# Kernel tuning notes

Hardware: AMD Instinct MI355X
Metric: run time of the kernel (lower is better)

The kernel has to match this reference:

```python
import jax, jax.numpy as jnp
import numpy as np
from jax import lax

ALPHA = 0.3  # SSGConv alpha


def _cdist(x):
    # Euclidean distance matrix [N, N] for x: [N, H]
    n2 = jnp.sum(x * x, axis=-1)
    d2 = n2[:, None] + n2[None, :] - 2.0 * (x @ x.T)
    return jnp.sqrt(jnp.maximum(d2, 0.0))


def _prim(dist):
    # Dense O(N^2) Prim MST starting at node 0. Returns (parents, children, weights), each [N-1].
    N = dist.shape[0]
    INF = jnp.float32(1e30)
    in_tree = jnp.zeros(N, dtype=bool).at[0].set(True)
    mind = dist[0]                       # best edge weight into tree per node
    parent = jnp.zeros(N, dtype=jnp.int32)

    def step(carry, _):
        in_tree, mind, parent = carry
        d = jnp.where(in_tree, INF, mind)
        v = jnp.argmin(d).astype(jnp.int32)
        w = d[v]
        p = parent[v]
        in_tree = in_tree.at[v].set(True)
        newd = dist[v]
        upd = newd < mind
        mind = jnp.where(upd, newd, mind)
        parent = jnp.where(upd, v, parent)
        return (in_tree, mind, parent), (p, v, w)

    _, (ps, vs, ws) = lax.scan(step, (in_tree, mind, parent), None, length=N - 1)
    return ps, vs, ws


def _build_edges(features):
    # Torch code detaches edge weights via .item(); mirror with stop_gradient.
    B, N, _ = features.shape
    dist = jax.vmap(_cdist)(lax.stop_gradient(features))   # [B, N, N]
    ps, vs, ws = jax.vmap(_prim)(dist)                     # each [B, N-1]
    off = (jnp.arange(B, dtype=jnp.int32) * N)[:, None]
    a = (ps + off).ravel()
    b = (vs + off).ravel()
    src = jnp.concatenate([a, b])   # MST edges are added in both directions
    dst = jnp.concatenate([b, a])
    ew = jnp.concatenate([ws.ravel(), ws.ravel()])
    return src, dst, ew


def _gcn_norm(src, dst, ew, num_nodes):
    # PyG gcn_norm: add self loops (weight 1), symmetric deg^-1/2 normalization.
    loop = jnp.arange(num_nodes, dtype=src.dtype)
    src = jnp.concatenate([src, loop])
    dst = jnp.concatenate([dst, loop])
    ew = jnp.concatenate([ew, jnp.ones(num_nodes, ew.dtype)])
    deg = jax.ops.segment_sum(ew, dst, num_segments=num_nodes)
    dinv = jnp.where(deg > 0, lax.rsqrt(jnp.maximum(deg, 1e-30)), 0.0)
    norm = dinv[src] * ew * dinv[dst]
    return src, dst, norm


def _ssg_conv(x, src, dst, norm, W, b, num_nodes):
    # SSGConv with K=1: h = alpha*x + (1-alpha)*A_hat x, then linear.
    prop = jax.ops.segment_sum(norm[:, None] * x[src], dst, num_segments=num_nodes)
    h = ALPHA * x + (1.0 - ALPHA) * prop
    return h @ W + b


def _forward(features, W1, b1, W2, b2, W3, b3, Wd, bd, Wo, bo):
    B, N, H = features.shape
    NT = B * N
    src, dst, ew = _build_edges(features)
    src, dst, norm = _gcn_norm(src, dst, ew, NT)
    x = features.reshape(NT, H)
    x = jnp.tanh(_ssg_conv(x, src, dst, norm, W1, b1, NT))
    x = jnp.tanh(_ssg_conv(x, src, dst, norm, W2, b2, NT))
    x = jnp.tanh(_ssg_conv(x, src, dst, norm, W3, b3, NT))
    # dropout: eval mode -> identity. global_mean_pool: each graph has exactly N nodes.
    pooled = x.reshape(B, N, -1).mean(axis=1)          # [B, 2H]
    h = jnp.tanh(pooled @ Wd + bd)                     # [B, H]
    return h @ Wo + bo                                 # [B, num_labels]


def setup_inputs() -> dict:
    key = jax.random.key(0)
    ks = jax.random.split(key, 12)
    B, N, H, L = 16, 1024, 256, 8
    H2 = 2 * H

    def lin(k, fin, fout):
        s = 1.0 / np.sqrt(fin)
        k1, k2 = jax.random.split(k)
        return (jax.random.uniform(k1, (fin, fout), jnp.float32, -s, s),
                jax.random.uniform(k2, (fout,), jnp.float32, -s, s))

    W1, b1 = lin(ks[1], H, H2)
    W2, b2 = lin(ks[2], H2, H2)
    W3, b3 = lin(ks[3], H2, H2)
    Wd, bd = lin(ks[4], H2, H)
    Wo, bo = lin(ks[5], H, L)
    features = jax.random.normal(ks[0], (B, N, H), jnp.float32)
    return {"features": features, "W1": W1, "b1": b1, "W2": W2, "b2": b2,
            "W3": W3, "b3": b3, "Wd": Wd, "bd": bd, "Wo": Wo, "bo": bo}


def reference(features, W1, b1, W2, b2, W3, b3, Wd, bd, Wo, bo):
    return _forward(features, W1, b1, W2, b2, W3, b3, Wd, bd, Wo, bo)
```

## Files before the change

### kernel.cpp

```cpp
#include <hip/hip_runtime.h>
#include <math.h>

namespace {

constexpr float ALPHA = 0.3f;
constexpr int B  = 16;
constexpr int N  = 1024;
constexpr int H  = 256;
constexpr int H2 = 512;
constexpr int NT = B * N;
constexpr int NE = N - 1;
constexpr int CAP = 32;

__device__ __forceinline__ unsigned umin32(unsigned a, unsigned b) { return a < b ? a : b; }

typedef __attribute__((ext_vector_type(8))) short short8;
typedef __attribute__((ext_vector_type(4))) float f32x4;

__global__ void n2_kernel(const float* __restrict__ x, float* __restrict__ n2) {
  int wave = threadIdx.x >> 6, lane = threadIdx.x & 63;
  int row  = blockIdx.x * 4 + wave;
  float4 v = *(const float4*)(x + (size_t)row * H + lane * 4);
  float s  = v.x * v.x + v.y * v.y + v.z * v.z + v.w * v.w;
  #pragma unroll
  for (int off = 32; off; off >>= 1) s += __shfl_xor(s, off);
  if (lane == 0) n2[row] = s;
}

__global__ __launch_bounds__(256) void dist_kernel(const float* __restrict__ x,
    const float* __restrict__ n2, float* __restrict__ dist) {
  __shared__ float As[16][132], Bs[16][132];
  const int bb = blockIdx.z;
  int idx = blockIdx.x, ti = 0;
  while (idx >= 8 - ti) { idx -= 8 - ti; ++ti; }
  const int tj = ti + idx;
  const int i0 = ti * 128, j0 = tj * 128;
  const int t = threadIdx.x, tx = t & 15, ty = t >> 4;
  const float* xb = x + (size_t)bb * N * H;
  float acc[8][8] = {};
  for (int kc = 0; kc < H; kc += 16) {
    #pragma unroll
    for (int u = 0; u < 2; ++u) {
      int q = t + u * 256;
      int row = q >> 2, kf = (q & 3) * 4;
      float4 a = *(const float4*)(xb + (size_t)(i0 + row) * H + kc + kf);
      As[kf + 0][row] = a.x; As[kf + 1][row] = a.y;
      As[kf + 2][row] = a.z; As[kf + 3][row] = a.w;
      float4 bv = *(const float4*)(xb + (size_t)(j0 + row) * H + kc + kf);
      Bs[kf + 0][row] = bv.x; Bs[kf + 1][row] = bv.y;
      Bs[kf + 2][row] = bv.z; Bs[kf + 3][row] = bv.w;
    }
    __syncthreads();
    #pragma unroll
    for (int kk = 0; kk < 16; ++kk) {
      float4 a0 = *(const float4*)&As[kk][ty * 4];
      float4 a1 = *(const float4*)&As[kk][64 + ty * 4];
      float4 b0 = *(const float4*)&Bs[kk][tx * 4];
      float4 b1 = *(const float4*)&Bs[kk][64 + tx * 4];
      float ar[8] = {a0.x,a0.y,a0.z,a0.w,a1.x,a1.y,a1.z,a1.w};
      float br[8] = {b0.x,b0.y,b0.z,b0.w,b1.x,b1.y,b1.z,b1.w};
      #pragma unroll
      for (int r = 0; r < 8; ++r)
        #pragma unroll
        for (int c = 0; c < 8; ++c) acc[r][c] += ar[r] * br[c];
    }
    __syncthreads();
  }
  float n2i[8], n2j[8];
  #pragma unroll
  for (int r = 0; r < 8; ++r)
    n2i[r] = n2[bb * N + i0 + (r < 4 ? ty * 4 + r : 64 + ty * 4 + r - 4)];
  #pragma unroll
  for (int c = 0; c < 8; ++c)
    n2j[c] = n2[bb * N + j0 + (c < 4 ? tx * 4 + c : 64 + tx * 4 + c - 4)];
  const bool mirror = (ti != tj);
  float* distb = dist + (size_t)bb * N * N;
  #pragma unroll
  for (int r = 0; r < 8; ++r) {
    int mi = i0 + (r < 4 ? ty * 4 + r : 64 + ty * 4 + r - 4);
    float o[8];
    #pragma unroll
    for (int c = 0; c < 8; ++c) {
      float d2 = (n2i[r] + n2j[c]) - 2.0f * acc[r][c];
      o[c] = sqrtf(fmaxf(d2, 0.0f));
    }
    float* dst = distb + (size_t)mi * N + j0;
    *(float4*)(dst + tx * 4)      = make_float4(o[0], o[1], o[2], o[3]);
    *(float4*)(dst + 64 + tx * 4) = make_float4(o[4], o[5], o[6], o[7]);
    if (mirror) {
      #pragma unroll
      for (int c = 0; c < 8; ++c) {
        int mj = j0 + (c < 4 ? tx * 4 + c : 64 + tx * 4 + c - 4);
        distb[(size_t)mj * N + mi] = o[c];
      }
    }
  }
}

__device__ __forceinline__ unsigned wave_min_u32(unsigned x) {
  unsigned t;
  t = (unsigned)__builtin_amdgcn_update_dpp((int)x, (int)x, 0x111, 0xf, 0xf, false); x = umin32(x, t);
  t = (unsigned)__builtin_amdgcn_update_dpp((int)x, (int)x, 0x112, 0xf, 0xf, false); x = umin32(x, t);
  t = (unsigned)__builtin_amdgcn_update_dpp((int)x, (int)x, 0x114, 0xf, 0xf, false); x = umin32(x, t);
  t = (unsigned)__builtin_amdgcn_update_dpp((int)x, (int)x, 0x118, 0xf, 0xf, false); x = umin32(x, t);
  x = umin32(x, (unsigned)__shfl_xor((int)x, 16));
  x = umin32(x, (unsigned)__shfl_xor((int)x, 32));
  return (unsigned)__builtin_amdgcn_readlane((int)x, 63);
}

struct Sel2 { unsigned w; int j; };

__device__ __forceinline__ Sel2 block_select(unsigned mw0, unsigned mw1,
    unsigned mw2, unsigned mw3, int wid, int lane, unsigned long long* smin) {
  unsigned lm = umin32(umin32(mw0, mw1), umin32(mw2, mw3));
  unsigned wm = wave_min_u32(lm);
  unsigned mb = (mw0 == wm ? 1u : 0u) | (mw1 == wm ? 2u : 0u) |
                (mw2 == wm ? 4u : 0u) | (mw3 == wm ? 8u : 0u);
  unsigned long long bal = __ballot(mb != 0);
  int fl = __ffsll(bal) - 1;
  int slot = __ffs((unsigned)__builtin_amdgcn_readlane((int)mb, fl)) - 1;
  int widx = (wid << 8) | (fl << 2) | slot;
  if (lane == 0)
    smin[wid] = ((unsigned long long)wm << 32) | (unsigned)widx;
  __syncthreads();
  unsigned long long k0 = smin[0], k1 = smin[1], k2 = smin[2], k3 = smin[3];
  unsigned long long ka = k0 < k1 ? k0 : k1;
  unsigned long long kb = k2 < k3 ? k2 : k3;
  unsigned long long kk = ka < kb ? ka : kb;
  __syncthreads();
  Sel2 r; r.w = (unsigned)(kk >> 32); r.j = (int)(unsigned)(kk & 0xFFFFFFFFu);
  return r;
}

__global__ __launch_bounds__(256) void prim_gemm1_kernel(
    const float* __restrict__ dist, const float* __restrict__ feat,
    const float* __restrict__ W1, int* __restrict__ ep, int* __restrict__ ev,
    float* __restrict__ ewt, float* __restrict__ y) {
  __shared__ unsigned long long smin[4];
  __shared__ int epv[NE];
  __shared__ int evv[NE];
  __shared__ float ews[NE];
  __shared__ float As[16][132], Bs[16][132];
  if (blockIdx.x < B) {
    const int b = blockIdx.x;
    const int tid = threadIdx.x, wid = tid >> 6, lane = tid & 63;
    const float* Db = dist + (size_t)b * N * N;
    const int jbase = tid * 4;

    unsigned d0, d1, d2, d3;
    {
      float4 v = *(const float4*)(Db + jbase);
      d0 = __float_as_uint(v.x); d1 = __float_as_uint(v.y);
      d2 = __float_as_uint(v.z); d3 = __float_as_uint(v.w);
    }
    unsigned mw0 = d0, mw1 = d1, mw2 = d2, mw3 = d3;
    unsigned rm0 = 0, rm1 = 0, rm2 = 0, rm3 = 0;
    int pa0 = 0, pa1 = 0, pa2 = 0, pa3 = 0;
    if (tid == 0) { rm0 = ~0u; mw0 = ~0u; }

    Sel2 s0 = block_select(mw0, mw1, mw2, mw3, wid, lane, smin);
    int cj = s0.j;
    if ((cj >> 2) == tid) {
      int sl = cj & 3;
      int pv = pa0; if (sl == 1) pv = pa1; if (sl == 2) pv = pa2; if (sl == 3) pv = pa3;
      epv[0] = pv; evv[0] = cj; ews[0] = __uint_as_float(s0.w);
      if (sl == 0) { rm0 = ~0u; mw0 = ~0u; }
      if (sl == 1) { rm1 = ~0u; mw1 = ~0u; }
      if (sl == 2) { rm2 = ~0u; mw2 = ~0u; }
      if (sl == 3) { rm3 = ~0u; mw3 = ~0u; }
    }
    float4 xq = *(const float4*)(Db + (size_t)cj * N + jbase);

    for (int k = 1; k < NE; ++k) {
      unsigned r0 = __float_as_uint(xq.x), r1 = __float_as_uint(xq.y);
      unsigned r2 = __float_as_uint(xq.z), r3 = __float_as_uint(xq.w);
      unsigned q0 = r0 | rm0, q1 = r1 | rm1, q2 = r2 | rm2, q3 = r3 | rm3;
      mw0 = umin32(mw0, q0); mw1 = umin32(mw1, q1);
      mw2 = umin32(mw2, q2); mw3 = umin32(mw3, q3);
      Sel2 se = block_select(mw0, mw1, mw2, mw3, wid, lane, smin);
      const int nj = se.j;
      float4 nxt = *(const float4*)(Db + (size_t)nj * N + jbase);
      if (r0 < d0) { pa0 = cj; d0 = r0; }
      if (r1 < d1) { pa1 = cj; d1 = r1; }
      if (r2 < d2) { pa2 = cj; d2 = r2; }
      if (r3 < d3) { pa3 = cj; d3 = r3; }
      if ((nj >> 2) == tid) {
        int sl = nj & 3;
        int pv = pa0; if (sl == 1) pv = pa1; if (sl == 2) pv = pa2; if (sl == 3) pv = pa3;
        epv[k] = pv; evv[k] = nj; ews[k] = __uint_as_float(se.w);
        if (sl == 0) { rm0 = ~0u; mw0 = ~0u; }
        if (sl == 1) { rm1 = ~0u; mw1 = ~0u; }
        if (sl == 2) { rm2 = ~0u; mw2 = ~0u; }
        if (sl == 3) { rm3 = ~0u; mw3 = ~0u; }
      }
      cj = nj; xq = nxt;
    }

    __syncthreads();
    for (int e = tid; e < NE; e += 256) {
      ep[b * NE + e]  = epv[e];
      ev[b * NE + e]  = evv[e];
      ewt[b * NE + e] = ews[e];
    }
  } else {
    const int gb = blockIdx.x - B;
    const int m0 = (gb >> 2) * 128, n0 = (gb & 3) * 128;
    const int t = threadIdx.x, tx = t & 15, ty = t >> 4;
    float acc[8][8] = {};
    for (int kc = 0; kc < H; kc += 16) {
      #pragma unroll
      for (int u = 0; u < 2; ++u) {
        int q = t + u * 256;
        int row = q >> 2, kf = (q & 3) * 4;
        float4 a = *(const float4*)(feat + (size_t)(m0 + row) * H + kc + kf);
        As[kf + 0][row] = a.x; As[kf + 1][row] = a.y;
        As[kf + 2][row] = a.z; As[kf + 3][row] = a.w;
        int rowB = q >> 5, cf = (q & 31) * 4;
        *(float4*)&Bs[rowB][cf] = *(const float4*)(W1 + (size_t)(kc + rowB) * H2 + n0 + cf);
      }
      __syncthreads();
      #pragma unroll
      for (int kk = 0; kk < 16; ++kk) {
        float4 a0 = *(const float4*)&As[kk][ty * 4];
        float4 a1 = *(const float4*)&As[kk][64 + ty * 4];
        float4 b0 = *(const float4*)&Bs[kk][tx * 4];
        float4 b1 = *(const float4*)&Bs[kk][64 + tx * 4];
        float ar[8] = {a0.x,a0.y,a0.z,a0.w,a1.x,a1.y,a1.z,a1.w};
        float br[8] = {b0.x,b0.y,b0.z,b0.w,b1.x,b1.y,b1.z,b1.w};
        #pragma unroll
        for (int r = 0; r < 8; ++r)
          #pragma unroll
          for (int c = 0; c < 8; ++c) acc[r][c] += ar[r] * br[c];
      }
      __syncthreads();
    }
    #pragma unroll
    for (int r = 0; r < 8; ++r) {
      int m = m0 + (r < 4 ? ty * 4 + r : 64 + ty * 4 + r - 4);
      float* dst = y + (size_t)m * H2 + n0;
      *(float4*)(dst + tx * 4)      = make_float4(acc[r][0], acc[r][1], acc[r][2], acc[r][3]);
      *(float4*)(dst + 64 + tx * 4) = make_float4(acc[r][4], acc[r][5], acc[r][6], acc[r][7]);
    }
  }
}

__global__ void adj_kernel(const int* __restrict__ ep, const int* __restrict__ ev,
    const float* __restrict__ ewt, int* __restrict__ adjI, float* __restrict__ adjW,
    int* __restrict__ cnt, float* __restrict__ dinv) {
  int i = blockIdx.x * 256 + threadIdx.x;
  int b = i >> 10, loc = i & 1023;
  const int* epb = ep + b * NE;
  const int* evb = ev + b * NE;
  const float* ewb = ewt + b * NE;
  int c = 0; float wsum = 0.0f;
  for (int k = 0; k < NE; ++k) {
    int p = epb[k], v = evb[k];
    if (p == loc || v == loc) {
      float w = ewb[k];
      wsum += w;
      int nb = (p == loc) ? v : p;
      if (c < CAP) { adjI[i * CAP + c] = (b << 10) + nb; adjW[i * CAP + c] = w; }
      ++c;
    }
  }
  cnt[i]  = c < CAP ? c : CAP;
  dinv[i] = 1.0f / sqrtf(wsum + 1.0f);
}

__global__ void finish1_kernel(const float* __restrict__ y, const int* __restrict__ adjI,
    const float* __restrict__ adjW, const int* __restrict__ cnt,
    const float* __restrict__ dinv, const float* __restrict__ b1,
    float* __restrict__ out1) {
  int wave = threadIdx.x >> 6, lane = threadIdx.x & 63;
  int i = blockIdx.x * 4 + wave;
  float dv = dinv[i];
  int c = cnt[i];
  float selfc = ALPHA + (1.0f - ALPHA) * dv * dv;
  float4 acc[2];
  const float* yi = y + (size_t)i * H2 + lane * 4;
  #pragma unroll
  for (int u = 0; u < 2; ++u) {
    float4 v = *(const float4*)(yi + u * 256);
    acc[u].x = selfc * v.x; acc[u].y = selfc * v.y;
    acc[u].z = selfc * v.z; acc[u].w = selfc * v.w;
  }
  for (int e = 0; e < c; ++e) {
    int j   = adjI[i * CAP + e];
    float w = adjW[i * CAP + e];
    float coef = (1.0f - ALPHA) * dv * (w * dinv[j]);
    const float* yj = y + (size_t)j * H2 + lane * 4;
    #pragma unroll
    for (int u = 0; u < 2; ++u) {
      float4 v = *(const float4*)(yj + u * 256);
      acc[u].x += coef * v.x; acc[u].y += coef * v.y;
      acc[u].z += coef * v.z; acc[u].w += coef * v.w;
    }
  }
  float* ho = out1 + (size_t)i * H2 + lane * 4;
  #pragma unroll
  for (int u = 0; u < 2; ++u) {
    float4 bb = *(const float4*)(b1 + lane * 4 + u * 256);
    float4 o;
    o.x = tanhf(acc[u].x + bb.x); o.y = tanhf(acc[u].y + bb.y);
    o.z = tanhf(acc[u].z + bb.z); o.w = tanhf(acc[u].w + bb.w);
    *(float4*)(ho + u * 256) = o;
  }
}

template <int HH>
__global__ void prop_kernel(const float* __restrict__ x, const int* __restrict__ adjI,
    const float* __restrict__ adjW, const int* __restrict__ cnt,
    const float* __restrict__ dinv, float* __restrict__ h) {
  constexpr int U = HH / 256;
  int wave = threadIdx.x >> 6, lane = threadIdx.x & 63;
  int i = blockIdx.x * 4 + wave;
  float dv = dinv[i];
  int c = cnt[i];
  float selfc = ALPHA + (1.0f - ALPHA) * dv * dv;
  float4 acc[U];
  const float* xi = x + (size_t)i * HH + lane * 4;
  #pragma unroll
  for (int u = 0; u < U; ++u) {
    float4 v = *(const float4*)(xi + u * 256);
    acc[u].x = selfc * v.x; acc[u].y = selfc * v.y;
    acc[u].z = selfc * v.z; acc[u].w = selfc * v.w;
  }
  for (int e = 0; e < c; ++e) {
    int j   = adjI[i * CAP + e];
    float w = adjW[i * CAP + e];
    float coef = (1.0f - ALPHA) * dv * (w * dinv[j]);
    const float* xj = x + (size_t)j * HH + lane * 4;
    #pragma unroll
    for (int u = 0; u < U; ++u) {
      float4 v = *(const float4*)(xj + u * 256);
      acc[u].x += coef * v.x; acc[u].y += coef * v.y;
      acc[u].z += coef * v.z; acc[u].w += coef * v.w;
    }
  }
  float* ho = h + (size_t)i * HH + lane * 4;
  #pragma unroll
  for (int u = 0; u < U; ++u) *(float4*)(ho + u * 256) = acc[u];
}

__device__ __forceinline__ void bf16split(float a, unsigned short& hi, unsigned short& lo) {
  unsigned u = __float_as_uint(a);
  hi = (unsigned short)(u >> 16);
  float fh = __uint_as_float(u & 0xFFFF0000u);
  float fl = a - fh;
  lo = (unsigned short)(__float_as_uint(fl) >> 16);
}

__global__ __launch_bounds__(256) void mgemm_tanh_kernel(const float* __restrict__ A,
    const float* __restrict__ W, const float* __restrict__ bias, float* __restrict__ C) {
  __shared__ unsigned short Ahi[128][40], Alo[128][40];
  __shared__ unsigned short Bhi[128][40], Blo[128][40];
  const int m0 = blockIdx.x * 128, n0 = blockIdx.y * 128;
  const int t = threadIdx.x;
  const int w = t >> 6, lane = t & 63;
  const int lrow = lane & 15, lk = (lane >> 4) * 8;
  f32x4 acc[2][8];
  #pragma unroll
  for (int mt = 0; mt < 2; ++mt)
    #pragma unroll
    for (int nt = 0; nt < 8; ++nt) acc[mt][nt] = (f32x4){0.f, 0.f, 0.f, 0.f};

  const int arow = t >> 1, akq = (t & 1) * 16;
  const int wr = t & 31, wc4 = (t >> 5) * 16;

  for (int kc = 0; kc < H2; kc += 32) {
    {
      const float* src = A + (size_t)(m0 + arow) * H2 + kc + akq;
      unsigned short h[16], l[16];
      #pragma unroll
      for (int i = 0; i < 16; i += 4) {
        float4 v = *(const float4*)(src + i);
        bf16split(v.x, h[i], l[i]);     bf16split(v.y, h[i+1], l[i+1]);
        bf16split(v.z, h[i+2], l[i+2]); bf16split(v.w, h[i+3], l[i+3]);
      }
      short8 ph0 = {(short)h[0],(short)h[1],(short)h[2],(short)h[3],
                    (short)h[4],(short)h[5],(short)h[6],(short)h[7]};
      short8 ph1 = {(short)h[8],(short)h[9],(short)h[10],(short)h[11],
                    (short)h[12],(short)h[13],(short)h[14],(short)h[15]};
      short8 pl0 = {(short)l[0],(short)l[1],(short)l[2],(short)l[3],
                    (short)l[4],(short)l[5],(short)l[6],(short)l[7]};
      short8 pl1 = {(short)l[8],(short)l[9],(short)l[10],(short)l[11],
                    (short)l[12],(short)l[13],(short)l[14],(short)l[15]};
      *(short8*)&Ahi[arow][akq]     = ph0;
      *(short8*)&Ahi[arow][akq + 8] = ph1;
      *(short8*)&Alo[arow][akq]     = pl0;
      *(short8*)&Alo[arow][akq + 8] = pl1;
    }
    {
      const float* wsrc = W + (size_t)(kc + wr) * H2 + n0 + wc4;
      #pragma unroll
      for (int i = 0; i < 16; i += 4) {
        float4 v = *(const float4*)(wsrc + i);
        unsigned short h0,h1,h2,h3,l0,l1,l2,l3;
        bf16split(v.x, h0, l0); bf16split(v.y, h1, l1);
        bf16split(v.z, h2, l2); bf16split(v.w, h3, l3);
        Bhi[wc4+i+0][wr] = h0; Bhi[wc4+i+1][wr] = h1;
        Bhi[wc4+i+2][wr] = h2; Bhi[wc4+i+3][wr] = h3;
        Blo[wc4+i+0][wr] = l0; Blo[wc4+i+1][wr] = l1;
        Blo[wc4+i+2][wr] = l2; Blo[wc4+i+3][wr] = l3;
      }
    }
    __syncthreads();
    const int r0 = w * 32 + lrow;
    short8 a0h = *(const short8*)&Ahi[r0][lk];
    short8 a0l = *(const short8*)&Alo[r0][lk];
    short8 a1h = *(const short8*)&Ahi[r0 + 16][lk];
    short8 a1l = *(const short8*)&Alo[r0 + 16][lk];
    #pragma unroll
    for (int nt = 0; nt < 8; ++nt) {
      short8 bh = *(const short8*)&Bhi[nt * 16 + lrow][lk];
      short8 bl = *(const short8*)&Blo[nt * 16 + lrow][lk];
      acc[0][nt] = __builtin_amdgcn_mfma_f32_16x16x32_bf16(a0h, bh, acc[0][nt], 0, 0, 0);
      acc[0][nt] = __builtin_amdgcn_mfma_f32_16x16x32_bf16(a0l, bh, acc[0][nt], 0, 0, 0);
      acc[0][nt] = __builtin_amdgcn_mfma_f32_16x16x32_bf16(a0h, bl, acc[0][nt], 0, 0, 0);
      acc[1][nt] = __builtin_amdgcn_mfma_f32_16x16x32_bf16(a1h, bh, acc[1][nt], 0, 0, 0);
      acc[1][nt] = __builtin_amdgcn_mfma_f32_16x16x32_bf16(a1l, bh, acc[1][nt], 0, 0, 0);
      acc[1][nt] = __builtin_amdgcn_mfma_f32_16x16x32_bf16(a1h, bl, acc[1][nt], 0, 0, 0);
    }
    __syncthreads();
  }
  #pragma unroll
  for (int mt = 0; mt < 2; ++mt) {
    #pragma unroll
    for (int nt = 0; nt < 8; ++nt) {
      int col = n0 + nt * 16 + lrow;
      float bcol = bias[col];
      #pragma unroll
      for (int i = 0; i < 4; ++i) {
        int row = m0 + w * 32 + mt * 16 + (lane >> 4) * 4 + i;
        C[(size_t)row * H2 + col] = tanhf(acc[mt][nt][i] + bcol);
      }
    }
  }
}

__global__ void pool_kernel(const float* __restrict__ x, float* __restrict__ pooled) {
  int b = blockIdx.x;
  int c = blockIdx.y * 256 + threadIdx.x;
  const float* xb = x + ((size_t)b << 10) * H2 + c;
  float s = 0.0f;
  for (int i = 0; i < N; ++i) s += xb[(size_t)i * H2];
  pooled[b * H2 + c] = s * (1.0f / N);
}

__global__ void head_kernel(const float* __restrict__ pooled, const float* __restrict__ Wd,
    const float* __restrict__ bd, const float* __restrict__ Wo, const float* __restrict__ bo,
    float* __restrict__ out) {
  __shared__ float sp[512], sh[256];
  int b = blockIdx.x, t = threadIdx.x;
  sp[t] = pooled[b * H2 + t];
  sp[t + 256] = pooled[b * H2 + t + 256];
  __syncthreads();
  float acc = bd[t];
  for (int c2 = 0; c2 < 512; ++c2) acc += sp[c2] * Wd[c2 * 256 + t];
  sh[t] = tanhf(acc);
  __syncthreads();
  if (t < 8) {
    float o = bo[t];
    for (int j = 0; j < 256; ++j) o += sh[j] * Wo[j * 8 + t];
    out[b * 8 + t] = o;
  }
}

}

extern "C" void kernel_launch(void* const* d_in, const int* in_sizes, int n_in,
                              void* d_out, int out_size, void* d_ws, size_t ws_size,
                              hipStream_t stream) {
  const float* feat = (const float*)d_in[0];
  const float* W1 = (const float*)d_in[1];
  const float* b1 = (const float*)d_in[2];
  const float* W2 = (const float*)d_in[3];
  const float* b2 = (const float*)d_in[4];
  const float* W3 = (const float*)d_in[5];
  const float* b3 = (const float*)d_in[6];
  const float* Wd = (const float*)d_in[7];
  const float* bd = (const float*)d_in[8];
  const float* Wo = (const float*)d_in[9];
  const float* bo = (const float*)d_in[10];
  float* out = (float*)d_out;
  char* ws = (char*)d_ws;

  float* dist = (float*)(ws);
  float* out1 = (float*)(ws);
  float* x2   = (float*)(ws + ((size_t)32 << 20));
  float* x3   = (float*)(ws);
  float* ybuf = (float*)(ws + ((size_t)64 << 20));
  float* hbuf = (float*)(ws + ((size_t)64 << 20));
  char* misc  = ws + ((size_t)96 << 20);
  int*   ep     = (int*)(misc);
  int*   ev     = (int*)(misc + 65536);
  float* ewt    = (float*)(misc + 131072);
  int*   cnt    = (int*)(misc + 196608);
  float* dinv   = (float*)(misc + 262144);
  int*   adjI   = (int*)(misc + 327680);
  float* adjW   = (float*)(misc + 327680 + 2097152);
  float* n2     = (float*)(misc + 327680 + 2 * 2097152);
  float* pooled = (float*)(misc + 327680 + 2 * 2097152 + 65536);

  n2_kernel<<<NT / 4, 256, 0, stream>>>(feat, n2);
  dist_kernel<<<dim3(36, 1, 16), 256, 0, stream>>>(feat, n2, dist);
  prim_gemm1_kernel<<<B + (NT / 128) * 4, 256, 0, stream>>>(
      dist, feat, W1, ep, ev, ewt, ybuf);
  adj_kernel<<<NT / 256, 256, 0, stream>>>(ep, ev, ewt, adjI, adjW, cnt, dinv);

  finish1_kernel<<<NT / 4, 256, 0, stream>>>(ybuf, adjI, adjW, cnt, dinv, b1, out1);
  prop_kernel<512><<<NT / 4, 256, 0, stream>>>(out1, adjI, adjW, cnt, dinv, hbuf);
  mgemm_tanh_kernel<<<dim3(NT / 128, 4), 256, 0, stream>>>(hbuf, W2, b2, x2);
  prop_kernel<512><<<NT / 4, 256, 0, stream>>>(x2, adjI, adjW, cnt, dinv, hbuf);
  mgemm_tanh_kernel<<<dim3(NT / 128, 4), 256, 0, stream>>>(hbuf, W3, b3, x3);

  pool_kernel<<<dim3(B, H2 / 256), 256, 0, stream>>>(x3, pooled);
  head_kernel<<<B, 256, 0, stream>>>(pooled, Wd, bd, Wo, bo, out);
}
```

Baseline: 1.093 ms.

## Transpose mirrored distance tiles through LDS and fuse adjacency build into Prim kernel

The distance kernel now stages each off-diagonal output tile in a single 128x136 shared buffer and writes the mirrored half as coalesced float4 rows, replacing scattered strided scalar stores. Separately, the Prim blocks build the adjacency list, counts and degree normalisation directly from their shared-memory edge arrays, which removes the edge-list round trip through global memory and the separate adjacency kernel launch. The trade-off is that only 16 blocks now do the O(N) adjacency scan, each thread handling four nodes serially, where previously 64 blocks covered it with one node per thread.

```diff
diff --git a/kernel.cpp b/kernel.cpp
--- a/kernel.cpp
+++ b/kernel.cpp
@@ -29,7 +29,7 @@
 
 __global__ __launch_bounds__(256) void dist_kernel(const float* __restrict__ x,
     const float* __restrict__ n2, float* __restrict__ dist) {
-  __shared__ float As[16][132], Bs[16][132];
+  __shared__ float sh[128][136];
   const int bb = blockIdx.z;
   int idx = blockIdx.x, ti = 0;
   while (idx >= 8 - ti) { idx -= 8 - ti; ++ti; }
@@ -44,19 +44,19 @@
       int q = t + u * 256;
       int row = q >> 2, kf = (q & 3) * 4;
       float4 a = *(const float4*)(xb + (size_t)(i0 + row) * H + kc + kf);
-      As[kf + 0][row] = a.x; As[kf + 1][row] = a.y;
-      As[kf + 2][row] = a.z; As[kf + 3][row] = a.w;
+      sh[kf + 0][row] = a.x; sh[kf + 1][row] = a.y;
+      sh[kf + 2][row] = a.z; sh[kf + 3][row] = a.w;
       float4 bv = *(const float4*)(xb + (size_t)(j0 + row) * H + kc + kf);
-      Bs[kf + 0][row] = bv.x; Bs[kf + 1][row] = bv.y;
-      Bs[kf + 2][row] = bv.z; Bs[kf + 3][row] = bv.w;
+      sh[16 + kf + 0][row] = bv.x; sh[16 + kf + 1][row] = bv.y;
+      sh[16 + kf + 2][row] = bv.z; sh[16 + kf + 3][row] = bv.w;
     }
     __syncthreads();
     #pragma unroll
     for (int kk = 0; kk < 16; ++kk) {
-      float4 a0 = *(const float4*)&As[kk][ty * 4];
-      float4 a1 = *(const float4*)&As[kk][64 + ty * 4];
-      float4 b0 = *(const float4*)&Bs[kk][tx * 4];
-      float4 b1 = *(const float4*)&Bs[kk][64 + tx * 4];
+      float4 a0 = *(const float4*)&sh[kk][ty * 4];
+      float4 a1 = *(const float4*)&sh[kk][64 + ty * 4];
+      float4 b0 = *(const float4*)&sh[16 + kk][tx * 4];
+      float4 b1 = *(const float4*)&sh[16 + kk][64 + tx * 4];
       float ar[8] = {a0.x,a0.y,a0.z,a0.w,a1.x,a1.y,a1.z,a1.w};
       float br[8] = {b0.x,b0.y,b0.z,b0.w,b1.x,b1.y,b1.z,b1.w};
       #pragma unroll
@@ -77,22 +77,33 @@
   float* distb = dist + (size_t)bb * N * N;
   #pragma unroll
   for (int r = 0; r < 8; ++r) {
-    int mi = i0 + (r < 4 ? ty * 4 + r : 64 + ty * 4 + r - 4);
+    int rl = (r < 4 ? ty * 4 + r : 64 + ty * 4 + r - 4);
     float o[8];
     #pragma unroll
     for (int c = 0; c < 8; ++c) {
       float d2 = (n2i[r] + n2j[c]) - 2.0f * acc[r][c];
       o[c] = sqrtf(fmaxf(d2, 0.0f));
     }
-    float* dst = distb + (size_t)mi * N + j0;
+    float* dst = distb + (size_t)(i0 + rl) * N + j0;
     *(float4*)(dst + tx * 4)      = make_float4(o[0], o[1], o[2], o[3]);
     *(float4*)(dst + 64 + tx * 4) = make_float4(o[4], o[5], o[6], o[7]);
     if (mirror) {
-      #pragma unroll
-      for (int c = 0; c < 8; ++c) {
-        int mj = j0 + (c < 4 ? tx * 4 + c : 64 + tx * 4 + c - 4);
-        distb[(size_t)mj * N + mi] = o[c];
-      }
+      *(float4*)&sh[rl][tx * 4]      = make_float4(o[0], o[1], o[2], o[3]);
+      *(float4*)&sh[rl][64 + tx * 4] = make_float4(o[4], o[5], o[6], o[7]);
+    }
+  }
+  if (mirror) {
+    __syncthreads();
+    const int q = t >> 1, half = (t & 1) * 64;
+    float* gdst = distb + (size_t)(j0 + q) * N + i0 + half;
+    #pragma unroll
+    for (int s = 0; s < 64; s += 4) {
+      float4 v;
+      v.x = sh[half + s + 0][q];
+      v.y = sh[half + s + 1][q];
+      v.z = sh[half + s + 2][q];
+      v.w = sh[half + s + 3][q];
+      *(float4*)(gdst + s) = v;
     }
   }
 }
@@ -134,8 +145,8 @@
 
 __global__ __launch_bounds__(256) void prim_gemm1_kernel(
     const float* __restrict__ dist, const float* __restrict__ feat,
-    const float* __restrict__ W1, int* __restrict__ ep, int* __restrict__ ev,
-    float* __restrict__ ewt, float* __restrict__ y) {
+    const float* __restrict__ W1, int* __restrict__ adjI, float* __restrict__ adjW,
+    int* __restrict__ cnt, float* __restrict__ dinv, float* __restrict__ y) {
   __shared__ unsigned long long smin[4];
   __shared__ int epv[NE];
   __shared__ int evv[NE];
@@ -197,10 +208,31 @@
     }
 
     __syncthreads();
-    for (int e = tid; e < NE; e += 256) {
-      ep[b * NE + e]  = epv[e];
-      ev[b * NE + e]  = evv[e];
-      ewt[b * NE + e] = ews[e];
+    {
+      const int base = b << 10;
+      const int l0 = jbase, l1 = jbase + 1, l2 = jbase + 2, l3 = jbase + 3;
+      int c0 = 0, c1 = 0, c2 = 0, c3 = 0;
+      float ws0 = 0.f, ws1 = 0.f, ws2 = 0.f, ws3 = 0.f;
+      for (int k = 0; k < NE; ++k) {
+        int p = epv[k], v = evv[k];
+        float w = ews[k];
+        if (p == l0 || v == l0) { ws0 += w; if (c0 < CAP) { int nb = (p == l0) ? v : p;
+            adjI[(size_t)(base + l0) * CAP + c0] = base + nb;
+            adjW[(size_t)(base + l0) * CAP + c0] = w; } ++c0; }
+        if (p == l1 || v == l1) { ws1 += w; if (c1 < CAP) { int nb = (p == l1) ? v : p;
+            adjI[(size_t)(base + l1) * CAP + c1] = base + nb;
+            adjW[(size_t)(base + l1) * CAP + c1] = w; } ++c1; }
+        if (p == l2 || v == l2) { ws2 += w; if (c2 < CAP) { int nb = (p == l2) ? v : p;
+            adjI[(size_t)(base + l2) * CAP + c2] = base + nb;
+            adjW[(size_t)(base + l2) * CAP + c2] = w; } ++c2; }
+        if (p == l3 || v == l3) { ws3 += w; if (c3 < CAP) { int nb = (p == l3) ? v : p;
+            adjI[(size_t)(base + l3) * CAP + c3] = base + nb;
+            adjW[(size_t)(base + l3) * CAP + c3] = w; } ++c3; }
+      }
+      cnt[base + l0] = c0 < CAP ? c0 : CAP;  dinv[base + l0] = 1.0f / sqrtf(ws0 + 1.0f);
+      cnt[base + l1] = c1 < CAP ? c1 : CAP;  dinv[base + l1] = 1.0f / sqrtf(ws1 + 1.0f);
+      cnt[base + l2] = c2 < CAP ? c2 : CAP;  dinv[base + l2] = 1.0f / sqrtf(ws2 + 1.0f);
+      cnt[base + l3] = c3 < CAP ? c3 : CAP;  dinv[base + l3] = 1.0f / sqrtf(ws3 + 1.0f);
     }
   } else {
     const int gb = blockIdx.x - B;
@@ -242,29 +274,6 @@
       *(float4*)(dst + 64 + tx * 4) = make_float4(acc[r][4], acc[r][5], acc[r][6], acc[r][7]);
     }
   }
-}
-
-__global__ void adj_kernel(const int* __restrict__ ep, const int* __restrict__ ev,
-    const float* __restrict__ ewt, int* __restrict__ adjI, float* __restrict__ adjW,
-    int* __restrict__ cnt, float* __restrict__ dinv) {
-  int i = blockIdx.x * 256 + threadIdx.x;
-  int b = i >> 10, loc = i & 1023;
-  const int* epb = ep + b * NE;
-  const int* evb = ev + b * NE;
-  const float* ewb = ewt + b * NE;
-  int c = 0; float wsum = 0.0f;
-  for (int k = 0; k < NE; ++k) {
-    int p = epb[k], v = evb[k];
-    if (p == loc || v == loc) {
-      float w = ewb[k];
-      wsum += w;
-      int nb = (p == loc) ? v : p;
-      if (c < CAP) { adjI[i * CAP + c] = (b << 10) + nb; adjW[i * CAP + c] = w; }
-      ++c;
-    }
-  }
-  cnt[i]  = c < CAP ? c : CAP;
-  dinv[i] = 1.0f / sqrtf(wsum + 1.0f);
 }
 
 __global__ void finish1_kernel(const float* __restrict__ y, const int* __restrict__ adjI,
@@ -492,9 +501,6 @@
   float* ybuf = (float*)(ws + ((size_t)64 << 20));
   float* hbuf = (float*)(ws + ((size_t)64 << 20));
   char* misc  = ws + ((size_t)96 << 20);
-  int*   ep     = (int*)(misc);
-  int*   ev     = (int*)(misc + 65536);
-  float* ewt    = (float*)(misc + 131072);
   int*   cnt    = (int*)(misc + 196608);
   float* dinv   = (float*)(misc + 262144);
   int*   adjI   = (int*)(misc + 327680);
@@ -505,8 +511,7 @@
   n2_kernel<<<NT / 4, 256, 0, stream>>>(feat, n2);
   dist_kernel<<<dim3(36, 1, 16), 256, 0, stream>>>(feat, n2, dist);
   prim_gemm1_kernel<<<B + (NT / 128) * 4, 256, 0, stream>>>(
-      dist, feat, W1, ep, ev, ewt, ybuf);
-  adj_kernel<<<NT / 256, 256, 0, stream>>>(ep, ev, ewt, adjI, adjW, cnt, dinv);
+      dist, feat, W1, adjI, adjW, cnt, dinv, ybuf);
 
   finish1_kernel<<<NT / 4, 256, 0, stream>>>(ybuf, adjI, adjW, cnt, dinv, b1, out1);
   prop_kernel<512><<<NT / 4, 256, 0, stream>>>(out1, adjI, adjW, cnt, dinv, hbuf);
```

Result: slower. 1.171 ms (+7.2%).
